# Performance work log

Measured on AMD Instinct MI355X. Metric: run time of the kernel, lower is better.

The kernel has to match this reference:

```python
import jax, jax.numpy as jnp
import numpy as np
import math

B = 2048
INPUT_SIZE = 1024
OUTPUT_SIZE = 512
SPONGE = 1024
ACT = 256
REC = 256
STORE = ACT + REC  # 512
DEPTH = 8
BDEPTH = 10
NEUTRAL_C = 1.0
SQRT2 = math.sqrt(2.0)


def _make_structure():
    # Deterministic stand-in for the module's random.sample-based recall wiring.
    rng = np.random.RandomState(0)
    half = (SPONGE + 1) // 2
    shuffle_perm = np.array([i // 2 + (i % 2) * half for i in range(SPONGE)], dtype=np.int64)
    unused = []
    recall = []
    for i in range(DEPTH):
        unused.extend(range(i * STORE, (i + 1) * STORE))
        sel = rng.choice(len(unused), size=REC, replace=False)
        sel_set = set(sel.tolist())
        recall.append([unused[k] for k in sorted(sel_set)])
        unused = [u for k, u in enumerate(unused) if k not in sel_set]
    out_mem = np.array(sorted(unused), dtype=np.int64)  # 2048 leftover memory columns
    bf_size = len(out_mem) + SPONGE  # 3072
    bf_depth = int(math.ceil(math.log2(bf_size)))  # 12
    bf_half = (bf_size + 1) // 2
    bf_perm = np.array([i // 2 + (i % 2) * bf_half for i in range(bf_size)], dtype=np.int64)
    return shuffle_perm, np.array(recall, dtype=np.int64), out_mem, bf_perm, bf_size, bf_depth


def setup_inputs() -> dict:
    key = jax.random.key(0)
    ks = jax.random.split(key, 6)
    shuffle_perm, recall_idx, out_mem_idx, bf_perm, bf_size, bf_depth = _make_structure()
    return {
        "X": jax.random.normal(ks[0], (B, INPUT_SIZE), jnp.float32),
        "scales": jnp.ones((INPUT_SIZE,), jnp.float32),
        "angles": jax.random.uniform(ks[1], (DEPTH, BDEPTH, SPONGE // 2), jnp.float32) * (2 * math.pi),
        "act_bias": jax.random.normal(ks[2], (DEPTH, ACT), jnp.float32),
        "act_activation": jax.random.normal(ks[3], (DEPTH, ACT), jnp.float32),
        "act_curvature": jax.random.normal(ks[4], (DEPTH, ACT), jnp.float32),
        "bf_angles": jax.random.uniform(ks[5], (bf_depth, bf_size // 2), jnp.float32) * (2 * math.pi),
        "shuffle_perm": jnp.asarray(shuffle_perm),
        "recall_idx": jnp.asarray(recall_idx),
        "output_mem_idx": jnp.asarray(out_mem_idx),
        "bf_perm": jnp.asarray(bf_perm),
    }


def _base_activation(x, c):
    # In the source, `a` is overwritten with torch.tensor(1.0), so a == 1.
    t = (math.pi / 4) / c
    y0 = (1.0 / c) * (1.0 / SQRT2 - math.cos(math.pi / 2))  # = 1/(c*sqrt(2))
    m0 = math.sin(math.pi / 2)  # = 1
    y1 = (1.0 / c) * (1.0 / SQRT2 - 1.0)
    m1 = math.sin(0.0)  # = 0
    mid = (1.0 / c) * (1.0 / SQRT2 - jnp.cos(math.pi / 4 + c * x))
    return jnp.where(x > t, y0 + m0 * (x - t), jnp.where(x < -t, y1 + m1 * (x + t), mid))


def _butterfly(x, angles, perm):
    # angles: [n_layers, exch]; shuffle -> Givens rotation per pair, extra passthrough
    exch = angles.shape[1]
    for j in range(angles.shape[0]):
        s = x[:, perm]
        x1, x2 = s[:, :exch], s[:, exch:2 * exch]
        ca, sa = jnp.cos(angles[j]), jnp.sin(angles[j])
        x = jnp.concatenate([ca * x1 + sa * x2, -sa * x1 + ca * x2, s[:, 2 * exch:]], axis=1)
    return x


def reference(X, scales, angles, act_bias, act_activation, act_curvature, bf_angles,
              shuffle_perm, recall_idx, output_mem_idx, bf_perm):
    Xs = X * scales
    sponge = Xs[:, :SPONGE]  # input_size == sponge_size: no zero pad, memory[0] is empty
    mem = jnp.zeros((Xs.shape[0], DEPTH * STORE), Xs.dtype)
    for i in range(DEPTH):
        sponge = _butterfly(sponge, angles[i], shuffle_perm)
        x1 = sponge[:, STORE:STORE + ACT] + act_bias[i]  # activation_position == store_size
        c = 0.5 * NEUTRAL_C * (act_curvature[i] + jnp.sqrt(act_curvature[i] ** 2 + 1.0))
        ap = _base_activation(x1, c)
        am = _base_activation(-x1, c)
        act_out = jnp.stack([ap, am], axis=2).reshape(ap.shape[0], 2 * ACT)  # interleave +/-
        mem = mem.at[:, i * STORE:(i + 1) * STORE].set(sponge[:, :STORE])
        recall = mem[:, recall_idx[i]]  # indices only address already-filled columns
        # [act_out | sponge[store:act_pos] (empty) | sponge[act_pos+ACT:] | recall]
        sponge = jnp.concatenate([act_out, sponge[:, STORE + ACT:], recall], axis=1)
    pre = jnp.concatenate([mem[:, output_mem_idx], sponge], axis=1)  # [B, 3072]
    out = _butterfly(pre, bf_angles, bf_perm)
    return out[:, :OUTPUT_SIZE]
```

## Files before the change

### kernel.cpp

```cpp
#include <hip/hip_runtime.h>
#include <math.h>

#define NB 2048
#define DEPTH 8

#define FTAB_OFF   0
#define BFT_OFF    81920
#define ACT4_OFF   118784
#define PHYS_OFF   126976
#define PHYSR_OFF  131072
#define PHYSO_OFF  133120
#define WS_FLOATS  135168

__global__ void tab_precompute(const float* __restrict__ angles,
                               const float* __restrict__ bf_angles,
                               const float* __restrict__ act_bias,
                               const float* __restrict__ act_curv,
                               float* __restrict__ ws) {
    int id = blockIdx.x * 256 + threadIdx.x;
    if (id < 40960) {
        int w  = id & 3;
        int t  = (id >> 2) & 255;
        int dg = id >> 10;
        int d = dg / 5, g = dg - 5 * d;
        int pA1 = 2 * (t & 127) + (t >> 7);
        int pair = (w == 0) ? pA1 : (w == 1) ? (pA1 + 256)
                 : (w == 2) ? (2 * pA1) : (2 * pA1 + 1);
        int st = 2 * g + (w >> 1);
        float a = angles[(d * 10 + st) * 512 + pair];
        float s, c; sincosf(a, &s, &c);
        ws[FTAB_OFF + 2 * id]     = c;
        ws[FTAB_OFF + 2 * id + 1] = s;
    } else if (id < 40960 + 18432) {
        int idb = id - 40960;
        float a = bf_angles[idb];
        float s, c; sincosf(a, &s, &c);
        ws[BFT_OFF + 2 * idb]     = c;
        ws[BFT_OFF + 2 * idb + 1] = s;
    } else if (id < 40960 + 18432 + 2048) {
        int ida = id - 59392;
        float cu = act_curv[ida];
        float c  = 0.5f * (cu + sqrtf(cu * cu + 1.0f));
        ((float4*)(ws + ACT4_OFF))[ida] =
            make_float4(act_bias[ida], c, 1.0f / c, 0.0f);
    }
}

__global__ void phys_precompute(const int* __restrict__ recall_idx,
                                const int* __restrict__ out_mem_idx,
                                float* __restrict__ ws) {
    __shared__ int physL[4096];
    int t = threadIdx.x;
    for (int q = 0; q < 4; ++q) {
        int v = t + q * 1024;
        int p;
        for (;;) {
            int d = v >> 9, j = v & 511;
            if (d == 0)  { p = j; break; }
            if (j < 256) { p = 256 + d * 256 + j; break; }
            v = recall_idx[(d - 1) * 256 + (j - 256)];
        }
        physL[t + q * 1024] = p;
        ((int*)(ws + PHYS_OFF))[t + q * 1024] = p;
    }
    __syncthreads();
    for (int q = 0; q < 2; ++q) {
        int i = t + q * 1024;
        ((int*)(ws + PHYSR_OFF))[i] = physL[recall_idx[i]];
        ((int*)(ws + PHYSO_OFF))[i] = physL[out_mem_idx[i]];
    }
}

__device__ __forceinline__ float actf(float x, float c, float ic) {
    const float is2 = 0.70710678118654752f;
    float tt = 0.78539816339744831f * ic;
    float y0 = is2 * ic;
    float y1 = (is2 - 1.0f) * ic;
    float mid = ic * (is2 - __cosf(0.78539816339744831f + c * x));
    return x > tt ? (y0 + (x - tt)) : (x < -tt ? y1 : mid);
}

__launch_bounds__(256, 8)
__global__ void sponge_kernel(const float* __restrict__ X,
                              const float* __restrict__ scales,
                              const float* __restrict__ ws,
                              float* __restrict__ out) {
    __shared__ float lds[4352];
    float* memb = lds;
    float* pb0  = lds + 2304;
    float* pb1  = lds + 3328;
    const int t   = threadIdx.x;
    const int row = blockIdx.x;

    const float* ftab = ws + FTAB_OFF;
    const float* bft  = ws + BFT_OFF;
    const float4* act4 = (const float4*)(ws + ACT4_OFF);
    const int* phys  = (const int*)(ws + PHYS_OFF);
    const int* physr = (const int*)(ws + PHYSR_OFF);
    const int* physo = (const int*)(ws + PHYSO_OFF);

    const int tl = t & 127, th = t >> 7;
    const int b  = tl + th * 512;
    const int a  = 2 * tl + th;

    float h0, h1, h2, h3;
    {
        const float* Xr = X + (size_t)row * 1024;
        h0 = Xr[b]       * scales[b];
        h1 = Xr[b + 128] * scales[b + 128];
        h2 = Xr[b + 256] * scales[b + 256];
        h3 = Xr[b + 384] * scales[b + 384];
    }

    float* wbuf = pb0;
    float* rbuf = pb1;

    for (int d = 0; d < DEPTH; ++d) {
        for (int g = 0; g < 5; ++g) {
            const float4* ft = (const float4*)(ftab + (size_t)((d * 5 + g) * 256 + t) * 8);
            float4 csA = ft[0];
            float4 csB = ft[1];
            float g0 =  csA.x * h0 + csA.y * h2;
            float g2 = -csA.y * h0 + csA.x * h2;
            float g1 =  csA.z * h1 + csA.w * h3;
            float g3 = -csA.w * h1 + csA.z * h3;
            float f0 =  csB.x * g0 + csB.y * g1;
            float f2 = -csB.y * g0 + csB.x * g1;
            float f1 =  csB.z * g2 + csB.w * g3;
            float f3 = -csB.w * g2 + csB.z * g3;
            ((float2*)(wbuf + 2 * a))[0]       = make_float2(f0, f1);
            ((float2*)(wbuf + 2 * a + 512))[0] = make_float2(f2, f3);
            { float* tmp = wbuf; wbuf = rbuf; rbuf = tmp; }
            __syncthreads();
            if (g < 4) {
                h0 = rbuf[b];
                h1 = rbuf[b + 128];
                h2 = rbuf[b + 256];
                h3 = rbuf[b + 384];
            }
        }
        const float* z = rbuf;
        {
            float2 mv = ((const float2*)(z + 2 * t))[0];
            int2  pm  = ((const int2*)(phys + d * 512))[t];
            memb[pm.x] = mv.x;
            memb[pm.y] = mv.y;
        }
        int r0 = 0, r1 = 0;
        if (t < 128) {
            int k0 = t >> 1;
            float x10 = z[512 + k0];
            float x11 = z[512 + k0 + 64];
            float x12 = z[512 + k0 + 128];
            float x13 = z[512 + k0 + 192];
            float4 a0 = act4[d * 256 + k0];
            float4 a1 = act4[d * 256 + k0 + 64];
            float4 a2 = act4[d * 256 + k0 + 128];
            float4 a3 = act4[d * 256 + k0 + 192];
            float sgn = (t & 1) ? -1.0f : 1.0f;
            h0 = actf(sgn * (x10 + a0.x), a0.y, a0.z);
            h1 = actf(sgn * (x11 + a1.x), a1.y, a1.z);
            h2 = actf(sgn * (x12 + a2.x), a2.y, a2.z);
            h3 = actf(sgn * (x13 + a3.x), a3.y, a3.z);
        } else {
            int u = t - 128;
            h0 = z[768 + u];
            h1 = z[896 + u];
            r0 = physr[d * 256 + u];
            r1 = physr[d * 256 + u + 128];
        }
        __syncthreads();
        if (t >= 128) {
            h2 = memb[r0];
            h3 = memb[r1];
        }
    }

    float gv[8];
#pragma unroll
    for (int q = 0; q < 8; ++q) gv[q] = memb[physo[q * 256 + t]];
    __syncthreads();
#pragma unroll
    for (int q = 0; q < 8; ++q) lds[q * 256 + t] = gv[q];
    lds[2048 + b]       = h0;
    lds[2048 + b + 128] = h1;
    lds[2048 + b + 256] = h2;
    lds[2048 + b + 384] = h3;
    __syncthreads();

    float* buf = lds;

    for (int s = 0; s < 3; ++s) {
        const float* tbs = bft + s * 3072;
        float  r[12];
        float4 csg[3];
#pragma unroll
        for (int gi = 0; gi < 3; ++gi) {
            csg[gi] = *(const float4*)(tbs + 4 * t + 1024 * gi);
            r[4 * gi + 0] = buf[t + 256 * gi];
            r[4 * gi + 1] = buf[t + 256 * gi + 768];
            r[4 * gi + 2] = buf[t + 256 * gi + 1536];
            r[4 * gi + 3] = buf[t + 256 * gi + 2304];
        }
        __syncthreads();
#pragma unroll
        for (int gi = 0; gi < 3; ++gi) {
            int j0 = 2 * t + 512 * gi;
            float4 cs = csg[gi];
            float av = r[4 * gi], bv = r[4 * gi + 1], cv = r[4 * gi + 2], ev = r[4 * gi + 3];
            ((float2*)(buf + j0))[0] =
                make_float2( cs.x * av + cs.y * bv,  cs.z * cv + cs.w * ev);
            ((float2*)(buf + 1536 + j0))[0] =
                make_float2(-cs.y * av + cs.x * bv, -cs.w * cv + cs.z * ev);
        }
        __syncthreads();
    }

#pragma unroll
    for (int s = 3; s < 11; ++s) {
        const float* tbs = bft + s * 3072;
        const int k  = 10 - s;
        const int M  = 768 >> k;
        const int Wl = 8 - k;
        const int Wm = (256 >> k) - 1;
        float  X1[2], X2[2];
        float2 cs2[2];
        int    pp[2];
#pragma unroll
        for (int u = 0; u < 2; ++u) {
            int i = t + 256 * u;
            int p = ((i >> Wl) * M) + (i & Wm);
            pp[u]  = p;
            cs2[u] = *(const float2*)(tbs + 2 * p);
            X1[u] = buf[(p >> 1) + (p & 1) * 1536];
            X2[u] = buf[768 + (p >> 1) + (p & 1) * 1536];
        }
        __syncthreads();
#pragma unroll
        for (int u = 0; u < 2; ++u) {
            buf[pp[u]]        =  cs2[u].x * X1[u] + cs2[u].y * X2[u];
            buf[pp[u] + 1536] = -cs2[u].y * X1[u] + cs2[u].x * X2[u];
        }
        __syncthreads();
    }

    {
        const float* tbs = bft + 11 * 3072;
        float4 cs = *(const float4*)(tbs + 4 * t);
        float av = buf[t], bv = buf[768 + t], cv = buf[1536 + t], ev = buf[2304 + t];
        ((float2*)(out + (size_t)row * 512))[t] =
            make_float2(cs.x * av + cs.y * bv, cs.z * cv + cs.w * ev);
    }
}

extern "C" void kernel_launch(void* const* d_in, const int* in_sizes, int n_in,
                              void* d_out, int out_size, void* d_ws, size_t ws_size,
                              hipStream_t stream) {
    const float* X          = (const float*)d_in[0];
    const float* scales     = (const float*)d_in[1];
    const float* angles     = (const float*)d_in[2];
    const float* act_bias   = (const float*)d_in[3];
    const float* act_curv   = (const float*)d_in[5];
    const float* bf_angles  = (const float*)d_in[6];
    const int*   recall_idx  = (const int*)d_in[8];
    const int*   out_mem_idx = (const int*)d_in[9];

    float* ws = (float*)d_ws;

    tab_precompute<<<240, 256, 0, stream>>>(angles, bf_angles, act_bias, act_curv, ws);
    phys_precompute<<<1, 1024, 0, stream>>>(recall_idx, out_mem_idx, ws);
    sponge_kernel<<<NB, 256, 0, stream>>>(X, scales, ws, (float*)d_out);
}
```

Baseline: 127.0 us.

## Fuse output butterfly stages in pairs, swizzle LDS layout, fold gather into first stages

The final 12-stage butterfly is restructured so that each thread applies two stages in registers per LDS round trip, halving the barrier and LDS traffic count. The output-memory gather is fused with the first two stages through a precomputed index table, so the gathered values go straight into registers instead of being staged through LDS. The depth-loop sponge buffer addresses are XOR-swizzled to reduce LDS bank conflicts. Twiddle tables are reorganised to match these paired-stage access patterns, which adds index complexity in the precompute kernels.

```diff
diff --git a/kernel.cpp b/kernel.cpp
--- a/kernel.cpp
+++ b/kernel.cpp
@@ -4,13 +4,13 @@
 #define NB 2048
 #define DEPTH 8
 
-#define FTAB_OFF   0
-#define BFT_OFF    81920
-#define ACT4_OFF   118784
-#define PHYS_OFF   126976
-#define PHYSR_OFF  131072
-#define PHYSO_OFF  133120
-#define WS_FLOATS  135168
+#define FTAB_OFF    0
+#define BF01_OFF    81920
+#define BFF_OFF     88064
+#define ACT4_OFF    98304
+#define PHYS_OFF    106496
+#define PHYSR_OFF   110592
+#define PHYSO2_OFF  112640
 
 __global__ void tab_precompute(const float* __restrict__ angles,
                                const float* __restrict__ bf_angles,
@@ -23,22 +23,41 @@
         int t  = (id >> 2) & 255;
         int dg = id >> 10;
         int d = dg / 5, g = dg - 5 * d;
-        int pA1 = 2 * (t & 127) + (t >> 7);
-        int pair = (w == 0) ? pA1 : (w == 1) ? (pA1 + 256)
-                 : (w == 2) ? (2 * pA1) : (2 * pA1 + 1);
+        int a = 2 * (t & 127) + (t >> 7);
+        int pair = (w == 0) ? a : (w == 1) ? (a + 256)
+                 : (w == 2) ? (2 * a) : (2 * a + 1);
         int st = 2 * g + (w >> 1);
-        float a = angles[(d * 10 + st) * 512 + pair];
-        float s, c; sincosf(a, &s, &c);
+        float ang = angles[(d * 10 + st) * 512 + pair];
+        float s, c; sincosf(ang, &s, &c);
         ws[FTAB_OFF + 2 * id]     = c;
         ws[FTAB_OFF + 2 * id + 1] = s;
-    } else if (id < 40960 + 18432) {
-        int idb = id - 40960;
-        float a = bf_angles[idb];
-        float s, c; sincosf(a, &s, &c);
-        ws[BFT_OFF + 2 * idb]     = c;
-        ws[BFT_OFF + 2 * idb + 1] = s;
-    } else if (id < 40960 + 18432 + 2048) {
-        int ida = id - 59392;
+    } else if (id < 44032) {
+        int e = id - 40960;
+        int w = e & 3; int ti = e >> 2;
+        int t = ti / 3; int i = ti - 3 * t;
+        int a = t + 256 * i;
+        int pair = (w == 0) ? a : (w == 1) ? (a + 768)
+                 : (w == 2) ? (2 * a) : (2 * a + 1);
+        int stage = (w < 2) ? 0 : 1;
+        float ang = bf_angles[stage * 1536 + pair];
+        float s, c; sincosf(ang, &s, &c);
+        ws[BF01_OFF + 2 * e]     = c;
+        ws[BF01_OFF + 2 * e + 1] = s;
+    } else if (id < 49152) {
+        int e = id - 44032;
+        int f = e >> 10; int rem = e & 1023; int t = rem >> 2; int w = rem & 3;
+        int P;
+        if (f == 0) P = 3 * t;
+        else { int k = 8 - 2 * f; P = ((t >> (2 * f)) * (768 >> k)) + (t & ((256 >> k) - 1)); }
+        int pair = (w == 0) ? P : (w == 1) ? (P + 768)
+                 : (w == 2) ? (2 * P) : (2 * P + 1);
+        int stage = (w < 2) ? (2 + 2 * f) : (3 + 2 * f);
+        float ang = bf_angles[stage * 1536 + pair];
+        float s, c; sincosf(ang, &s, &c);
+        ws[BFF_OFF + 2 * e]     = c;
+        ws[BFF_OFF + 2 * e + 1] = s;
+    } else if (id < 51200) {
+        int ida = id - 49152;
         float cu = act_curv[ida];
         float c  = 0.5f * (cu + sqrtf(cu * cu + 1.0f));
         ((float4*)(ws + ACT4_OFF))[ida] =
@@ -67,7 +86,14 @@
     for (int q = 0; q < 2; ++q) {
         int i = t + q * 1024;
         ((int*)(ws + PHYSR_OFF))[i] = physL[recall_idx[i]];
-        ((int*)(ws + PHYSO_OFF))[i] = physL[out_mem_idx[i]];
+    }
+    for (int e = t; e < 3072; e += 1024) {
+        int tt = e / 12; int r = e - 12 * tt; int i = r >> 2; int k = r & 3;
+        int a = tt + 256 * i;
+        int tl = a >> 1, th = a & 1;
+        int pos = tl + 1536 * th + 384 * k;
+        int val = (pos < 2048) ? physL[out_mem_idx[pos]] : (2304 + (pos - 2048));
+        ((int*)(ws + PHYSO2_OFF))[e] = val;
     }
 }
 
@@ -78,6 +104,11 @@
     float y1 = (is2 - 1.0f) * ic;
     float mid = ic * (is2 - __cosf(0.78539816339744831f + c * x));
     return x > tt ? (y0 + (x - tt)) : (x < -tt ? y1 : mid);
+}
+
+__device__ __forceinline__ int swz(int p) {
+    return (p & 1) | ((p & 0x3C) >> 1) | ((((p >> 6) ^ (p >> 1)) & 1) << 5)
+         | (((p >> 1) & 1) << 6) | (p & 0x380);
 }
 
 __launch_bounds__(256, 8)
@@ -92,16 +123,29 @@
     const int t   = threadIdx.x;
     const int row = blockIdx.x;
 
-    const float* ftab = ws + FTAB_OFF;
-    const float* bft  = ws + BFT_OFF;
-    const float4* act4 = (const float4*)(ws + ACT4_OFF);
-    const int* phys  = (const int*)(ws + PHYS_OFF);
-    const int* physr = (const int*)(ws + PHYSR_OFF);
-    const int* physo = (const int*)(ws + PHYSO_OFF);
+    const float4* bf01  = (const float4*)(ws + BF01_OFF);
+    const float4* bff   = (const float4*)(ws + BFF_OFF);
+    const float4* act4  = (const float4*)(ws + ACT4_OFF);
+    const int* phys   = (const int*)(ws + PHYS_OFF);
+    const int* physr  = (const int*)(ws + PHYSR_OFF);
+    const int* physo2 = (const int*)(ws + PHYSO2_OFF);
 
     const int tl = t & 127, th = t >> 7;
     const int b  = tl + th * 512;
     const int a  = 2 * tl + th;
+
+    const int wA0 = swz(2 * a), wA1 = swz(2 * a + 512);
+    const int rd0 = swz(b), rd1 = swz(b + 128), rd2 = swz(b + 256), rd3 = swz(b + 384);
+    const int zmem = swz(2 * t);
+    const int u = t - 128;
+    int za0 = 0, za1 = 0, za2 = 0, za3 = 0, zk0 = 0, zk1 = 0;
+    if (t < 128) {
+        int k0 = t >> 1;
+        za0 = swz(512 + k0);       za1 = swz(512 + k0 + 64);
+        za2 = swz(512 + k0 + 128); za3 = swz(512 + k0 + 192);
+    } else {
+        zk0 = swz(768 + u); zk1 = swz(896 + u);
+    }
 
     float h0, h1, h2, h3;
     {
@@ -114,12 +158,11 @@
 
     float* wbuf = pb0;
     float* rbuf = pb1;
+    const float4* ft = (const float4*)(ws + FTAB_OFF) + 2 * t;
 
     for (int d = 0; d < DEPTH; ++d) {
         for (int g = 0; g < 5; ++g) {
-            const float4* ft = (const float4*)(ftab + (size_t)((d * 5 + g) * 256 + t) * 8);
-            float4 csA = ft[0];
-            float4 csB = ft[1];
+            float4 csA = ft[0], csB = ft[1]; ft += 512;
             float g0 =  csA.x * h0 + csA.y * h2;
             float g2 = -csA.y * h0 + csA.x * h2;
             float g1 =  csA.z * h1 + csA.w * h3;
@@ -128,31 +171,23 @@
             float f2 = -csB.y * g0 + csB.x * g1;
             float f1 =  csB.z * g2 + csB.w * g3;
             float f3 = -csB.w * g2 + csB.z * g3;
-            ((float2*)(wbuf + 2 * a))[0]       = make_float2(f0, f1);
-            ((float2*)(wbuf + 2 * a + 512))[0] = make_float2(f2, f3);
+            *(float2*)(wbuf + wA0) = make_float2(f0, f1);
+            *(float2*)(wbuf + wA1) = make_float2(f2, f3);
             { float* tmp = wbuf; wbuf = rbuf; rbuf = tmp; }
             __syncthreads();
             if (g < 4) {
-                h0 = rbuf[b];
-                h1 = rbuf[b + 128];
-                h2 = rbuf[b + 256];
-                h3 = rbuf[b + 384];
+                h0 = rbuf[rd0]; h1 = rbuf[rd1]; h2 = rbuf[rd2]; h3 = rbuf[rd3];
             }
         }
         const float* z = rbuf;
-        {
-            float2 mv = ((const float2*)(z + 2 * t))[0];
-            int2  pm  = ((const int2*)(phys + d * 512))[t];
-            memb[pm.x] = mv.x;
-            memb[pm.y] = mv.y;
-        }
+        float2 mv = *(const float2*)(z + zmem);
+        int2 pm = ((const int2*)(phys + d * 512))[t];
+        memb[pm.x] = mv.x;
+        memb[pm.y] = mv.y;
         int r0 = 0, r1 = 0;
         if (t < 128) {
+            float x10 = z[za0], x11 = z[za1], x12 = z[za2], x13 = z[za3];
             int k0 = t >> 1;
-            float x10 = z[512 + k0];
-            float x11 = z[512 + k0 + 64];
-            float x12 = z[512 + k0 + 128];
-            float x13 = z[512 + k0 + 192];
             float4 a0 = act4[d * 256 + k0];
             float4 a1 = act4[d * 256 + k0 + 64];
             float4 a2 = act4[d * 256 + k0 + 128];
@@ -163,9 +198,8 @@
             h2 = actf(sgn * (x12 + a2.x), a2.y, a2.z);
             h3 = actf(sgn * (x13 + a3.x), a3.y, a3.z);
         } else {
-            int u = t - 128;
-            h0 = z[768 + u];
-            h1 = z[896 + u];
+            h0 = z[zk0];
+            h1 = z[zk1];
             r0 = physr[d * 256 + u];
             r1 = physr[d * 256 + u + 128];
         }
@@ -176,80 +210,76 @@
         }
     }
 
-    float gv[8];
+    lds[2304 + b]       = h0;
+    lds[2304 + b + 128] = h1;
+    lds[2304 + b + 256] = h2;
+    lds[2304 + b + 384] = h3;
+    __syncthreads();
+    int4 pg0 = ((const int4*)(physo2 + t * 12))[0];
+    int4 pg1 = ((const int4*)(physo2 + t * 12))[1];
+    int4 pg2 = ((const int4*)(physo2 + t * 12))[2];
+    float v[12];
+    v[0] = lds[pg0.x]; v[1]  = lds[pg0.y]; v[2]  = lds[pg0.z]; v[3]  = lds[pg0.w];
+    v[4] = lds[pg1.x]; v[5]  = lds[pg1.y]; v[6]  = lds[pg1.z]; v[7]  = lds[pg1.w];
+    v[8] = lds[pg2.x]; v[9]  = lds[pg2.y]; v[10] = lds[pg2.z]; v[11] = lds[pg2.w];
+    __syncthreads();
+    float* buf = lds;
 #pragma unroll
-    for (int q = 0; q < 8; ++q) gv[q] = memb[physo[q * 256 + t]];
+    for (int i = 0; i < 3; ++i) {
+        float4 c01 = bf01[(t * 3 + i) * 2];
+        float4 c23 = bf01[(t * 3 + i) * 2 + 1];
+        float q0 = v[4 * i], q1 = v[4 * i + 1], q2 = v[4 * i + 2], q3 = v[4 * i + 3];
+        float g0 =  c01.x * q0 + c01.y * q2;
+        float g2 = -c01.y * q0 + c01.x * q2;
+        float g1 =  c01.z * q1 + c01.w * q3;
+        float g3 = -c01.w * q1 + c01.z * q3;
+        float y0 =  c23.x * g0 + c23.y * g1;
+        float y2 = -c23.y * g0 + c23.x * g1;
+        float y1 =  c23.z * g2 + c23.w * g3;
+        float y3 = -c23.w * g2 + c23.z * g3;
+        *(float2*)(buf + 2 * t + 512 * i)        = make_float2(y0, y1);
+        *(float2*)(buf + 2 * t + 512 * i + 1536) = make_float2(y2, y3);
+    }
     __syncthreads();
+
 #pragma unroll
-    for (int q = 0; q < 8; ++q) lds[q * 256 + t] = gv[q];
-    lds[2048 + b]       = h0;
-    lds[2048 + b + 128] = h1;
-    lds[2048 + b + 256] = h2;
-    lds[2048 + b + 384] = h3;
-    __syncthreads();
-
-    float* buf = lds;
-
-    for (int s = 0; s < 3; ++s) {
-        const float* tbs = bft + s * 3072;
-        float  r[12];
-        float4 csg[3];
-#pragma unroll
-        for (int gi = 0; gi < 3; ++gi) {
-            csg[gi] = *(const float4*)(tbs + 4 * t + 1024 * gi);
-            r[4 * gi + 0] = buf[t + 256 * gi];
-            r[4 * gi + 1] = buf[t + 256 * gi + 768];
-            r[4 * gi + 2] = buf[t + 256 * gi + 1536];
-            r[4 * gi + 3] = buf[t + 256 * gi + 2304];
-        }
+    for (int f = 0; f < 4; ++f) {
+        int P;
+        if (f == 0) P = 3 * t;
+        else { const int k = 8 - 2 * f;
+               P = ((t >> (2 * f)) * (768 >> k)) + (t & ((256 >> k) - 1)); }
+        int base = (P >> 1) + (P & 1) * 1536;
+        float4 csS = bff[(f * 256 + t) * 2];
+        float4 csT = bff[(f * 256 + t) * 2 + 1];
+        float x1p = buf[base], x1q = buf[base + 384];
+        float x2p = buf[base + 768], x2q = buf[base + 1152];
+        float o1P =  csS.x * x1p + csS.y * x2p;
+        float o2P = -csS.y * x1p + csS.x * x2p;
+        float o1Q =  csS.z * x1q + csS.w * x2q;
+        float o2Q = -csS.w * x1q + csS.z * x2q;
+        float y0 =  csT.x * o1P + csT.y * o1Q;
+        float y2 = -csT.y * o1P + csT.x * o1Q;
+        float y1 =  csT.z * o2P + csT.w * o2Q;
+        float y3 = -csT.w * o2P + csT.z * o2Q;
         __syncthreads();
-#pragma unroll
-        for (int gi = 0; gi < 3; ++gi) {
-            int j0 = 2 * t + 512 * gi;
-            float4 cs = csg[gi];
-            float av = r[4 * gi], bv = r[4 * gi + 1], cv = r[4 * gi + 2], ev = r[4 * gi + 3];
-            ((float2*)(buf + j0))[0] =
-                make_float2( cs.x * av + cs.y * bv,  cs.z * cv + cs.w * ev);
-            ((float2*)(buf + 1536 + j0))[0] =
-                make_float2(-cs.y * av + cs.x * bv, -cs.w * cv + cs.z * ev);
-        }
+        *(float2*)(buf + 2 * P)        = make_float2(y0, y1);
+        *(float2*)(buf + 2 * P + 1536) = make_float2(y2, y3);
         __syncthreads();
     }
 
-#pragma unroll
-    for (int s = 3; s < 11; ++s) {
-        const float* tbs = bft + s * 3072;
-        const int k  = 10 - s;
-        const int M  = 768 >> k;
-        const int Wl = 8 - k;
-        const int Wm = (256 >> k) - 1;
-        float  X1[2], X2[2];
-        float2 cs2[2];
-        int    pp[2];
-#pragma unroll
-        for (int u = 0; u < 2; ++u) {
-            int i = t + 256 * u;
-            int p = ((i >> Wl) * M) + (i & Wm);
-            pp[u]  = p;
-            cs2[u] = *(const float2*)(tbs + 2 * p);
-            X1[u] = buf[(p >> 1) + (p & 1) * 1536];
-            X2[u] = buf[768 + (p >> 1) + (p & 1) * 1536];
-        }
-        __syncthreads();
-#pragma unroll
-        for (int u = 0; u < 2; ++u) {
-            buf[pp[u]]        =  cs2[u].x * X1[u] + cs2[u].y * X2[u];
-            buf[pp[u] + 1536] = -cs2[u].y * X1[u] + cs2[u].x * X2[u];
-        }
-        __syncthreads();
-    }
-
     {
-        const float* tbs = bft + 11 * 3072;
-        float4 cs = *(const float4*)(tbs + 4 * t);
-        float av = buf[t], bv = buf[768 + t], cv = buf[1536 + t], ev = buf[2304 + t];
-        ((float2*)(out + (size_t)row * 512))[t] =
-            make_float2(cs.x * av + cs.y * bv, cs.z * cv + cs.w * ev);
+        int base = (t >> 1) + (t & 1) * 1536;
+        float4 csS = bff[(4 * 256 + t) * 2];
+        float4 csT = bff[(4 * 256 + t) * 2 + 1];
+        float x1p = buf[base], x1q = buf[base + 384];
+        float x2p = buf[base + 768], x2q = buf[base + 1152];
+        float o1P =  csS.x * x1p + csS.y * x2p;
+        float o2P = -csS.y * x1p + csS.x * x2p;
+        float o1Q =  csS.z * x1q + csS.w * x2q;
+        float o2Q = -csS.w * x1q + csS.z * x2q;
+        float y0 = csT.x * o1P + csT.y * o1Q;
+        float y1 = csT.z * o2P + csT.w * o2Q;
+        *(float2*)(out + (size_t)row * 512 + 2 * t) = make_float2(y0, y1);
     }
 }
 
@@ -267,7 +297,7 @@
 
     float* ws = (float*)d_ws;
 
-    tab_precompute<<<240, 256, 0, stream>>>(angles, bf_angles, act_bias, act_curv, ws);
+    tab_precompute<<<200, 256, 0, stream>>>(angles, bf_angles, act_bias, act_curv, ws);
     phys_precompute<<<1, 1024, 0, stream>>>(recall_idx, out_mem_idx, ws);
     sponge_kernel<<<NB, 256, 0, stream>>>(X, scales, ws, (float*)d_out);
 }
```

Result: slower. 135.6 us (+6.7%).
